# Performance work log

Measured on AMD Instinct MI355X. Metric: run time of the kernel, lower is better.

## Reference

```python
import jax, jax.numpy as jnp
import numpy as np

T, B, C = 1024, 8, 1024
H, K, P = 16, 7, 3  # num_heads, kernel_size, padding_l
R = C // H


def setup_inputs() -> dict:
    key = jax.random.key(0)
    k1, k2, k3, k4 = jax.random.split(key, 4)
    x = jax.random.normal(k1, (T, B, C), dtype=jnp.float32)
    # weight_linear: Linear(C -> H*K) with bias
    lim = 1.0 / np.sqrt(C)
    W_lin = jax.random.uniform(k2, (H * K, C), minval=-lim, maxval=lim, dtype=jnp.float32)
    b_lin = jax.random.uniform(k3, (H * K,), minval=-lim, maxval=lim, dtype=jnp.float32)
    conv_bias = jnp.zeros((C,), dtype=jnp.float32)
    return {"x": x, "W_lin": W_lin, "b_lin": b_lin, "conv_bias": conv_bias}


def reference(x, W_lin, b_lin, conv_bias):
    # per-position dynamic filters: (T, B, H*K)
    w = jnp.einsum('tbc,oc->tbo', x, W_lin) + b_lin
    # weight_softmax=True, renorm_padding=False: softmax over kernel dim
    w = jax.nn.softmax(w.reshape(T * B * H, K), axis=-1)
    # (T, B*H, K) -> (B*H, T, K)
    w = w.reshape(T, B * H, K).transpose(1, 0, 2)
    # x as (B*H, T, R)
    xv = x.reshape(T, B * H, R).transpose(1, 0, 2)
    # band-matrix bmm == sliding window: out[t] = sum_k w[t,k] * x[t - P + k]
    x_pad = jnp.pad(xv, ((0, 0), (P, K - 1 - P), (0, 0)))
    windows = jnp.stack([x_pad[:, k:k + T] for k in range(K)], axis=2)  # (BH, T, K, R)
    out = jnp.einsum('btk,btkr->btr', w, windows)  # (BH, T, R)
    out = out.transpose(1, 0, 2).reshape(T, B, C)
    return out + conv_bias[None, None, :]
```

## Files before the change

### kernel.cpp

```cpp
#include <hip/hip_runtime.h>
#include <stdint.h>

#define T_DIM 1024
#define B_DIM 8
#define C_DIM 1024
#define H_DIM 16
#define K_SZ  7
#define P_PAD 3
#define O_DIM (H_DIM * K_SZ)
#define TB    (T_DIM * B_DIM)

typedef __attribute__((ext_vector_type(8))) short bf16x8;
typedef __attribute__((ext_vector_type(4))) float f32x4;
typedef __attribute__((ext_vector_type(2))) uint32_t u32x2;

union FragU { uint32_t u[4]; bf16x8 v; };

__device__ inline uint32_t pk_bf16(float a, float b) {
  uint32_t ua = __float_as_uint(a), ub = __float_as_uint(b);
  ua += 0x7FFFu + ((ua >> 16) & 1u);
  ub += 0x7FFFu + ((ub >> 16) & 1u);
  return (ua >> 16) | (ub & 0xFFFF0000u);
}

__device__ inline bf16x8 load_bf16x8_cvt(const float* __restrict__ p) {
  float4 lo = *reinterpret_cast<const float4*>(p);
  float4 hi = *reinterpret_cast<const float4*>(p + 4);
  FragU f;
  f.u[0] = pk_bf16(lo.x, lo.y);
  f.u[1] = pk_bf16(lo.z, lo.w);
  f.u[2] = pk_bf16(hi.x, hi.y);
  f.u[3] = pk_bf16(hi.z, hi.w);
  return f.v;
}

__global__ __launch_bounds__(256) void prep_wfrag_kernel(
    const float* __restrict__ Wl, uint16_t* __restrict__ Wf) {
  const int t  = blockIdx.x * 256 + threadIdx.x;
  const int f  = t >> 6;
  const int l  = t & 63;
  const int ks = f / 7;
  const int nf = f - ks * 7;
  const int row = nf * 16 + (l & 15);
  const int kb  = ks * 32 + (l >> 4) * 8;
  bf16x8 v = load_bf16x8_cvt(Wl + (size_t)row * C_DIM + kb);
  *reinterpret_cast<bf16x8*>(Wf + (size_t)t * 8) = v;
}

template <bool PREPPED>
__global__ __launch_bounds__(256) void fused_dynconv_kernel(
    const float* __restrict__ x, const float* __restrict__ Wl,
    const uint16_t* __restrict__ Wf, const float* __restrict__ bl,
    const float* __restrict__ cb, float* __restrict__ out) {
  __shared__ char buf[4 * 8192];
  __shared__ float w_s[16][113];

  const int tid  = threadIdx.x;
  const int wv   = tid >> 6;
  const int lane = tid & 63;
  const int l15  = lane & 15;
  const int oct  = lane >> 4;
  const int bid  = blockIdx.x;
  const int swz  = (bid & 7) * 64 + (bid >> 3);
  const int rb   = swz * 16;
  const int kw   = wv * 256;
  char* lds = buf + wv * 8192;

  {
    const float* __restrict__ xs = x + (size_t)rb * C_DIM + kw;
#pragma unroll
    for (int r = 0; r < 16; ++r) {
      float4 v = *reinterpret_cast<const float4*>(xs + (size_t)r * C_DIM + lane * 4);
      u32x2 d;
      d.x = pk_bf16(v.x, v.y);
      d.y = pk_bf16(v.z, v.w);
      int byte = r * 512 + ((lane * 8) ^ ((r & 7) << 4));
      *reinterpret_cast<u32x2*>(lds + byte) = d;
    }
  }
  __syncthreads();

  f32x4 acc[7];
#pragma unroll
  for (int nf = 0; nf < 7; ++nf) acc[nf] = (f32x4)(0.f);

#pragma unroll
  for (int ks = 0; ks < 8; ++ks) {
    const int abyte = l15 * 512 + (((oct * 16) + ks * 64) ^ ((l15 & 7) << 4));
    bf16x8 a = *reinterpret_cast<const bf16x8*>(lds + abyte);
#pragma unroll
    for (int nf = 0; nf < 7; ++nf) {
      bf16x8 b;
      if (PREPPED) {
        b = *reinterpret_cast<const bf16x8*>(
            Wf + ((size_t)(((wv * 8 + ks) * 7 + nf) * 64) + lane) * 8);
      } else {
        b = load_bf16x8_cvt(Wl + (size_t)(nf * 16 + l15) * C_DIM + kw + ks * 32 + oct * 8);
      }
      acc[nf] = __builtin_amdgcn_mfma_f32_16x16x32_bf16(a, b, acc[nf], 0, 0, 0);
    }
  }

  {
    float* part = reinterpret_cast<float*>(lds);
#pragma unroll
    for (int nf = 0; nf < 7; ++nf)
#pragma unroll
      for (int r = 0; r < 4; ++r)
        part[(oct * 4 + r) * 116 + nf * 16 + l15] = acc[nf][r];
  }
  __syncthreads();

  {
    const int row = tid >> 4;
    const int h   = tid & 15;
    float lg[7];
    float m = -1e30f;
#pragma unroll
    for (int j = 0; j < 7; ++j) {
      const int c = h * 7 + j;
      const int o = row * 116 + c;
      float sum = reinterpret_cast<float*>(buf)[o]
                + reinterpret_cast<float*>(buf + 8192)[o]
                + reinterpret_cast<float*>(buf + 16384)[o]
                + reinterpret_cast<float*>(buf + 24576)[o] + bl[c];
      lg[j] = sum;
      m = fmaxf(m, sum);
    }
    float s = 0.f;
#pragma unroll
    for (int j = 0; j < 7; ++j) { lg[j] = __expf(lg[j] - m); s += lg[j]; }
    const float inv = 1.0f / s;
#pragma unroll
    for (int j = 0; j < 7; ++j) w_s[row][h * 7 + j] = lg[j] * inv;
  }
  __syncthreads();

  {
    const int row = tid >> 4;
    const int t15 = tid & 15;
    const int rg  = rb + row;
    const int tt  = rg >> 3;
    const int bb  = rg & 7;
    const float* __restrict__ wrow = &w_s[row][0];

    size_t xoff[7];
    bool ok[7];
#pragma unroll
    for (int j = 0; j < 7; ++j) {
      int tp = tt + j - P_PAD;
      ok[j] = (tp >= 0) && (tp < T_DIM);
      int tpc = min(max(tp, 0), T_DIM - 1);
      xoff[j] = (size_t)(tpc * B_DIM + bb) * C_DIM;
    }

#pragma unroll 4
    for (int i = 0; i < 16; ++i) {
      const int ch = i * 64 + t15 * 4;
      float4 a4 = *reinterpret_cast<const float4*>(cb + ch);
#pragma unroll
      for (int j = 0; j < 7; ++j) {
        float wj = ok[j] ? wrow[i * 7 + j] : 0.f;
        float4 xv = *reinterpret_cast<const float4*>(x + xoff[j] + ch);
        a4.x += wj * xv.x;
        a4.y += wj * xv.y;
        a4.z += wj * xv.z;
        a4.w += wj * xv.w;
      }
      *reinterpret_cast<float4*>(out + (size_t)rg * C_DIM + ch) = a4;
    }
  }
}

extern "C" void kernel_launch(void* const* d_in, const int* in_sizes, int n_in,
                              void* d_out, int out_size, void* d_ws, size_t ws_size,
                              hipStream_t stream) {
  const float* x  = (const float*)d_in[0];
  const float* Wl = (const float*)d_in[1];
  const float* bl = (const float*)d_in[2];
  const float* cb = (const float*)d_in[3];
  float* out = (float*)d_out;

  const size_t WF_BYTES = 262144;
  const bool prepped = ws_size >= WF_BYTES;

  if (prepped) {
    uint16_t* wf = (uint16_t*)d_ws;
    prep_wfrag_kernel<<<(32 * 7 * 64) / 256, 256, 0, stream>>>(Wl, wf);
    fused_dynconv_kernel<true><<<TB / 16, 256, 0, stream>>>(x, Wl, wf, bl, cb, out);
  } else {
    fused_dynconv_kernel<false><<<TB / 16, 256, 0, stream>>>(x, Wl, nullptr, bl, cb, out);
  }
}
```

Before: 30.26 us.

## Tile blocks by time per batch and reuse bf16 x halo in LDS for conv

Each block now covers 16 consecutive time steps of a single batch. It stages the 22-row halo of x, converted to bf16, into swizzled LDS. The sliding-window convolution then reads x from LDS instead of re-reading it seven times from global memory. The GEMM is also re-split so each wave owns one or two N-fragments across the full K=1024, which removes the cross-wave partial-sum reduction. The convolution now uses bf16-rounded x rather than fp32, which lowers accuracy, and it needs about 44KB of LDS per block, which may reduce occupancy.

```diff
diff --git a/kernel.cpp b/kernel.cpp
--- a/kernel.cpp
+++ b/kernel.cpp
@@ -12,7 +12,7 @@
 
 typedef __attribute__((ext_vector_type(8))) short bf16x8;
 typedef __attribute__((ext_vector_type(4))) float f32x4;
-typedef __attribute__((ext_vector_type(2))) uint32_t u32x2;
+typedef __attribute__((ext_vector_type(4))) uint32_t u32x4;
 
 union FragU { uint32_t u[4]; bf16x8 v; };
 
@@ -52,62 +52,79 @@
     const float* __restrict__ x, const float* __restrict__ Wl,
     const uint16_t* __restrict__ Wf, const float* __restrict__ bl,
     const float* __restrict__ cb, float* __restrict__ out) {
-  __shared__ char buf[4 * 8192];
-  __shared__ float w_s[16][113];
+  __shared__ char  xbf[22 * 2048];
+  __shared__ float part[16][116];
+  __shared__ float wsm[16][17][8];
 
   const int tid  = threadIdx.x;
   const int wv   = tid >> 6;
   const int lane = tid & 63;
   const int l15  = lane & 15;
   const int oct  = lane >> 4;
-  const int bid  = blockIdx.x;
-  const int swz  = (bid & 7) * 64 + (bid >> 3);
-  const int rb   = swz * 16;
-  const int kw   = wv * 256;
-  char* lds = buf + wv * 8192;
-
-  {
-    const float* __restrict__ xs = x + (size_t)rb * C_DIM + kw;
-#pragma unroll
-    for (int r = 0; r < 16; ++r) {
-      float4 v = *reinterpret_cast<const float4*>(xs + (size_t)r * C_DIM + lane * 4);
-      u32x2 d;
-      d.x = pk_bf16(v.x, v.y);
-      d.y = pk_bf16(v.z, v.w);
-      int byte = r * 512 + ((lane * 8) ^ ((r & 7) << 4));
-      *reinterpret_cast<u32x2*>(lds + byte) = d;
+
+  const int bid    = blockIdx.x;
+  const int w8     = bid >> 3;
+  const int t_tile = (bid & 7) * 8 + (w8 & 7);
+  const int b      = w8 >> 3;
+  const int t0     = t_tile * 16;
+
+  {
+#pragma unroll
+    for (int it = 0; it < 11; ++it) {
+      const int task = tid + it * 256;
+      const int q    = task >> 7;
+      const int c16  = task & 127;
+      const int trow = min(max(t0 + q - P_PAD, 0), T_DIM - 1);
+      const float* __restrict__ src =
+          x + ((size_t)(trow * B_DIM + b)) * C_DIM + c16 * 8;
+      float4 v0 = *reinterpret_cast<const float4*>(src);
+      float4 v1 = *reinterpret_cast<const float4*>(src + 4);
+      FragU f;
+      f.u[0] = pk_bf16(v0.x, v0.y);
+      f.u[1] = pk_bf16(v0.z, v0.w);
+      f.u[2] = pk_bf16(v1.x, v1.y);
+      f.u[3] = pk_bf16(v1.z, v1.w);
+      const int dst = q * 2048 + ((c16 * 16) ^ ((q & 7) << 4));
+      *reinterpret_cast<bf16x8*>(xbf + dst) = f.v;
     }
   }
   __syncthreads();
 
-  f32x4 acc[7];
-#pragma unroll
-  for (int nf = 0; nf < 7; ++nf) acc[nf] = (f32x4)(0.f);
-
-#pragma unroll
-  for (int ks = 0; ks < 8; ++ks) {
-    const int abyte = l15 * 512 + (((oct * 16) + ks * 64) ^ ((l15 & 7) << 4));
-    bf16x8 a = *reinterpret_cast<const bf16x8*>(lds + abyte);
-#pragma unroll
-    for (int nf = 0; nf < 7; ++nf) {
-      bf16x8 b;
+  {
+    const int nf0 = wv * 2;
+    const int nfc = (wv == 3) ? 1 : 2;
+    f32x4 acc0 = (f32x4)(0.f), acc1 = (f32x4)(0.f);
+    const int arow  = 3 + l15;
+    const int abase = arow * 2048;
+    const int axor  = (arow & 7) << 4;
+#pragma unroll
+    for (int ks = 0; ks < 32; ++ks) {
+      bf16x8 a = *reinterpret_cast<const bf16x8*>(
+          xbf + abase + ((ks * 64 + oct * 16) ^ axor));
+      bf16x8 b0, b1;
       if (PREPPED) {
-        b = *reinterpret_cast<const bf16x8*>(
-            Wf + ((size_t)(((wv * 8 + ks) * 7 + nf) * 64) + lane) * 8);
+        b0 = *reinterpret_cast<const bf16x8*>(
+            Wf + ((size_t)((ks * 7 + nf0) * 64) + lane) * 8);
+        if (nfc == 2)
+          b1 = *reinterpret_cast<const bf16x8*>(
+              Wf + ((size_t)((ks * 7 + nf0 + 1) * 64) + lane) * 8);
       } else {
-        b = load_bf16x8_cvt(Wl + (size_t)(nf * 16 + l15) * C_DIM + kw + ks * 32 + oct * 8);
+        b0 = load_bf16x8_cvt(Wl + (size_t)(nf0 * 16 + l15) * C_DIM + ks * 32 + oct * 8);
+        if (nfc == 2)
+          b1 = load_bf16x8_cvt(Wl + (size_t)((nf0 + 1) * 16 + l15) * C_DIM + ks * 32 + oct * 8);
       }
-      acc[nf] = __builtin_amdgcn_mfma_f32_16x16x32_bf16(a, b, acc[nf], 0, 0, 0);
-    }
-  }
-
-  {
-    float* part = reinterpret_cast<float*>(lds);
-#pragma unroll
-    for (int nf = 0; nf < 7; ++nf)
+      acc0 = __builtin_amdgcn_mfma_f32_16x16x32_bf16(a, b0, acc0, 0, 0, 0);
+      if (nfc == 2)
+        acc1 = __builtin_amdgcn_mfma_f32_16x16x32_bf16(a, b1, acc1, 0, 0, 0);
+    }
+#pragma unroll
+    for (int r = 0; r < 4; ++r)
+      part[oct * 4 + r][nf0 * 16 + l15] = acc0[r];
+    if (nfc == 2) {
 #pragma unroll
       for (int r = 0; r < 4; ++r)
-        part[(oct * 4 + r) * 116 + nf * 16 + l15] = acc[nf][r];
+        part[oct * 4 + r][(nf0 + 1) * 16 + l15] = acc1[r];
+    }
   }
   __syncthreads();
 
@@ -118,56 +135,59 @@
     float m = -1e30f;
 #pragma unroll
     for (int j = 0; j < 7; ++j) {
-      const int c = h * 7 + j;
-      const int o = row * 116 + c;
-      float sum = reinterpret_cast<float*>(buf)[o]
-                + reinterpret_cast<float*>(buf + 8192)[o]
-                + reinterpret_cast<float*>(buf + 16384)[o]
-                + reinterpret_cast<float*>(buf + 24576)[o] + bl[c];
-      lg[j] = sum;
-      m = fmaxf(m, sum);
+      float s_ = part[row][h * 7 + j] + bl[h * 7 + j];
+      lg[j] = s_;
+      m = fmaxf(m, s_);
     }
     float s = 0.f;
 #pragma unroll
     for (int j = 0; j < 7; ++j) { lg[j] = __expf(lg[j] - m); s += lg[j]; }
     const float inv = 1.0f / s;
 #pragma unroll
-    for (int j = 0; j < 7; ++j) w_s[row][h * 7 + j] = lg[j] * inv;
+    for (int j = 0; j < 7; ++j) wsm[row][h][j] = lg[j] * inv;
   }
   __syncthreads();
 
   {
-    const int row = tid >> 4;
-    const int t15 = tid & 15;
-    const int rg  = rb + row;
-    const int tt  = rg >> 3;
-    const int bb  = rg & 7;
-    const float* __restrict__ wrow = &w_s[row][0];
-
-    size_t xoff[7];
-    bool ok[7];
+    const int row   = tid >> 4;
+    const int t15   = tid & 15;
+    const int tglob = t0 + row;
+    float okf[7];
 #pragma unroll
     for (int j = 0; j < 7; ++j) {
-      int tp = tt + j - P_PAD;
-      ok[j] = (tp >= 0) && (tp < T_DIM);
-      int tpc = min(max(tp, 0), T_DIM - 1);
-      xoff[j] = (size_t)(tpc * B_DIM + bb) * C_DIM;
-    }
-
-#pragma unroll 4
-    for (int i = 0; i < 16; ++i) {
-      const int ch = i * 64 + t15 * 4;
-      float4 a4 = *reinterpret_cast<const float4*>(cb + ch);
+      int tp = tglob + j - P_PAD;
+      okf[j] = (tp >= 0 && tp < T_DIM) ? 1.f : 0.f;
+    }
+    float* __restrict__ obase = out + ((size_t)(tglob * B_DIM + b)) * C_DIM;
+
+#pragma unroll
+    for (int ii = 0; ii < 8; ++ii) {
+      const int ch0  = ii * 128 + t15 * 8;
+      const int head = ii * 2 + (t15 >> 3);
+      float4 w0 = *reinterpret_cast<const float4*>(&wsm[row][head][0]);
+      float4 w1 = *reinterpret_cast<const float4*>(&wsm[row][head][4]);
+      const float wj[7] = {w0.x, w0.y, w0.z, w0.w, w1.x, w1.y, w1.z};
+      float4 c0 = *reinterpret_cast<const float4*>(cb + ch0);
+      float4 c1 = *reinterpret_cast<const float4*>(cb + ch0 + 4);
+      float a0 = c0.x, a1 = c0.y, a2 = c0.z, a3 = c0.w;
+      float a4 = c1.x, a5 = c1.y, a6 = c1.z, a7 = c1.w;
 #pragma unroll
       for (int j = 0; j < 7; ++j) {
-        float wj = ok[j] ? wrow[i * 7 + j] : 0.f;
-        float4 xv = *reinterpret_cast<const float4*>(x + xoff[j] + ch);
-        a4.x += wj * xv.x;
-        a4.y += wj * xv.y;
-        a4.z += wj * xv.z;
-        a4.w += wj * xv.w;
+        const float w = wj[j] * okf[j];
+        const int q = row + j;
+        const u32x4 d = *reinterpret_cast<const u32x4*>(
+            xbf + q * 2048 + ((ii * 256 + t15 * 16) ^ ((q & 7) << 4)));
+        a0 += w * __uint_as_float(d.x << 16);
+        a1 += w * __uint_as_float(d.x & 0xffff0000u);
+        a2 += w * __uint_as_float(d.y << 16);
+        a3 += w * __uint_as_float(d.y & 0xffff0000u);
+        a4 += w * __uint_as_float(d.z << 16);
+        a5 += w * __uint_as_float(d.z & 0xffff0000u);
+        a6 += w * __uint_as_float(d.w << 16);
+        a7 += w * __uint_as_float(d.w & 0xffff0000u);
       }
-      *reinterpret_cast<float4*>(out + (size_t)rg * C_DIM + ch) = a4;
+      *reinterpret_cast<float4*>(obase + ch0)     = make_float4(a0, a1, a2, a3);
+      *reinterpret_cast<float4*>(obase + ch0 + 4) = make_float4(a4, a5, a6, a7);
     }
   }
 }
@@ -181,8 +201,7 @@
   const float* cb = (const float*)d_in[3];
   float* out = (float*)d_out;
 
-  const size_t WF_BYTES = 262144;
-  const bool prepped = ws_size >= WF_BYTES;
+  const bool prepped = ws_size >= 262144;
 
   if (prepped) {
     uint16_t* wf = (uint16_t*)d_ws;
```

Measured after the change: 33.25 us. 1.1x slower.
